# Kernel optimization log

Hardware: AMD Instinct MI355X
Metric: run time of the kernel (lower is better)

## Reference

```python
import math
import jax, jax.numpy as jnp
import numpy as np

CHANNELS = 1024
N_HEADS = 16
WINDOW = 4

def _get_relative_embeddings(emb, length, window):
    # emb: [n_heads_rel, 2*window+1, k_channels]
    pad_len = max(length - (window + 1), 0)
    start = max(window + 1 - length, 0)
    if pad_len > 0:
        emb = jnp.pad(emb, ((0, 0), (pad_len, pad_len), (0, 0)), mode='edge')
    return emb[:, start:start + 2 * length - 1]  # [n_rel, 2L-1, kc]

def _rel_to_abs(x):
    # x: [b, h, t, 2t-1] -> [b, h, t, t] via pad/reshape shift trick
    b, h, t, _ = x.shape
    x = jnp.pad(x, ((0, 0), (0, 0), (0, 0), (0, 1)))          # [b,h,t,2t]
    x = x.reshape(b, h, t * 2 * t)
    x = jnp.pad(x, ((0, 0), (0, 0), (0, t - 1)))
    x = x.reshape(b, h, t + 1, 2 * t - 1)
    return x[:, :, :t, t - 1:]

def setup_inputs() -> dict:
    key = jax.random.key(0)
    ks = jax.random.split(key, 12)
    B, C, T = 8, CHANNELS, 1024
    kc = C // N_HEADS
    sc = 1.0 / math.sqrt(C)
    inp = {
        'x': jax.random.normal(ks[0], (B, C, T), jnp.float32),
        'c': jax.random.normal(ks[1], (B, C, T), jnp.float32),
        'wq': jax.random.normal(ks[2], (C, C), jnp.float32) * sc,
        'bq': jnp.zeros((C,), jnp.float32),
        'wk': jax.random.normal(ks[3], (C, C), jnp.float32) * sc,
        'bk': jnp.zeros((C,), jnp.float32),
        'wv': jax.random.normal(ks[4], (C, C), jnp.float32) * sc,
        'bv': jnp.zeros((C,), jnp.float32),
        'wo': jax.random.normal(ks[5], (C, C), jnp.float32) * sc,
        'bo': jnp.zeros((C,), jnp.float32),
        'emb_rel_k': jax.random.normal(ks[6], (1, 2 * WINDOW + 1, kc), jnp.float32) * kc ** -0.5,
        'emb_rel_v': jax.random.normal(ks[7], (1, 2 * WINDOW + 1, kc), jnp.float32) * kc ** -0.5,
    }
    return inp

def reference(x, c, wq, bq, wk, bk, wv, bv, wo, bo, emb_rel_k, emb_rel_v):
    b, d, t = x.shape
    h = N_HEADS
    kc = d // h
    # 1x1 conv == pointwise linear over channels
    q = jnp.einsum('oc,bct->bot', wq, x) + bq[None, :, None]
    k = jnp.einsum('oc,bct->bot', wk, c) + bk[None, :, None]
    v = jnp.einsum('oc,bct->bot', wv, c) + bv[None, :, None]
    qh = q.reshape(b, h, kc, t)
    kh = k.reshape(b, h, kc, t)
    vh = v.reshape(b, h, kc, t)
    scale = 1.0 / math.sqrt(kc)
    scores = jnp.einsum('bhct,bhcs->bhts', qh * scale, kh)  # [b,h,t,t]
    # relative position bias on keys (heads_share=True -> n_rel=1 broadcast)
    rel_k = _get_relative_embeddings(emb_rel_k, t, WINDOW)  # [1, 2t-1, kc]
    rel_logits = jnp.einsum('bhct,nmc->bhtm', qh * scale, rel_k)  # [b,h,t,2t-1]
    scores = scores + _rel_to_abs(rel_logits)
    p_attn = jax.nn.softmax(scores, axis=-1)
    out = jnp.einsum('bhts,bhcs->bhct', p_attn, vh).reshape(b, d, t)
    out = jnp.einsum('oc,bct->bot', wo, out) + bo[None, :, None]
    return out
```

## Files before the change

kernel.cpp:

```cpp
#include <hip/hip_runtime.h>
#include <stdint.h>


#define DI __device__ __forceinline__

typedef float f32x4 __attribute__((ext_vector_type(4)));
typedef short short4v __attribute__((ext_vector_type(4)));
typedef short short8v __attribute__((ext_vector_type(8)));
typedef int int2v __attribute__((ext_vector_type(2)));
typedef _Float16 f16x4 __attribute__((ext_vector_type(4)));
typedef _Float16 f16x8 __attribute__((ext_vector_type(8)));

DI f32x4 mfma32(short8v a, short8v b, f32x4 c) {
  return __builtin_amdgcn_mfma_f32_16x16x32_f16(
      __builtin_bit_cast(f16x8, a), __builtin_bit_cast(f16x8, b), c, 0, 0, 0);
}
DI f32x4 mfma16x(short4v a, short4v b, f32x4 c) {
  return __builtin_amdgcn_mfma_f32_16x16x16f16(
      __builtin_bit_cast(f16x4, a), __builtin_bit_cast(f16x4, b), c, 0, 0, 0);
}

DI short f2h(float x) {
  _Float16 h = (_Float16)x;
  return __builtin_bit_cast(short, h);
}

DI short4v pack4(float p0, float p1, float p2, float p3) {
  auto a = __builtin_amdgcn_cvt_pkrtz(p0, p1);
  auto b = __builtin_amdgcn_cvt_pkrtz(p2, p3);
  int2v iv;
  iv[0] = __builtin_bit_cast(int, a);
  iv[1] = __builtin_bit_cast(int, b);
  return __builtin_bit_cast(short4v, iv);
}

DI int swz(int r) { return (r ^ (r >> 2)) & 3; }

DI void gl_lds16(const void* g, void* l) {
  __builtin_amdgcn_global_load_lds(
      (const __attribute__((address_space(1))) unsigned int*)g,
      (__attribute__((address_space(3))) unsigned int*)l, 16, 0, 0);
}

__global__ __launch_bounds__(256) void k_pre(
    const float* __restrict__ x, const float* __restrict__ c,
    const float* __restrict__ wq, const float* __restrict__ wk,
    const float* __restrict__ wv, const float* __restrict__ wo,
    short* __restrict__ Wall, short* __restrict__ xT, short* __restrict__ cT) {
  __shared__ float tile[64][65];
  int l = blockIdx.x;
  int tid = threadIdx.x;
  if (l < 4096) {
    int bx = l & 15, by = (l >> 4) & 15, bz = l >> 8;
    const float* src = (bz < 8 ? x : c) + (size_t)(bz & 7) * 1048576;
    short* dst = (bz < 8 ? xT : cT) + (size_t)(bz & 7) * 1048576;
    int t0 = bx * 64, c0 = by * 64;
    int tx = tid & 15, ty = tid >> 4;
#pragma unroll
    for (int rr_ = 0; rr_ < 64; rr_ += 16) {
      int r = rr_ + ty;
      f32x4 v = *(const f32x4*)(src + (size_t)(c0 + r) * 1024 + t0 + tx * 4);
      tile[r][tx * 4 + 0] = v[0]; tile[r][tx * 4 + 1] = v[1];
      tile[r][tx * 4 + 2] = v[2]; tile[r][tx * 4 + 3] = v[3];
    }
    __syncthreads();
#pragma unroll
    for (int rr_ = 0; rr_ < 64; rr_ += 16) {
      int r = rr_ + ty;
      short4v o;
      o[0] = f2h(tile[tx * 4 + 0][r]); o[1] = f2h(tile[tx * 4 + 1][r]);
      o[2] = f2h(tile[tx * 4 + 2][r]); o[3] = f2h(tile[tx * 4 + 3][r]);
      *(short4v*)(dst + (size_t)(t0 + r) * 1024 + c0 + tx * 4) = o;
    }
  } else {
    int l2 = l - 4096;
    int y = l2 >> 10, bx = l2 & 1023;
    const float* src = (y == 0) ? wq : (y == 1) ? wk : (y == 2) ? wv : wo;
    int i = (bx * 256 + tid) * 4;
    f32x4 v = *(const f32x4*)(src + i);
    short4v o;
    o[0] = f2h(v[0]); o[1] = f2h(v[1]); o[2] = f2h(v[2]); o[3] = f2h(v[3]);
    *(short4v*)(Wall + (size_t)y * 1048576 + i) = o;
  }
}

__global__ __launch_bounds__(256, 4) void k_proj(
    const short* __restrict__ Wall, const short* __restrict__ xT,
    const short* __restrict__ cT, const short* __restrict__ aT,
    const float* __restrict__ bq, const float* __restrict__ bk,
    const float* __restrict__ bv, const float* __restrict__ bo,
    short* __restrict__ QT, short* __restrict__ KT, short* __restrict__ Vv,
    float* __restrict__ outO, int zbase) {
  int z = blockIdx.z + zbase;
  int p = z >> 3, b = z & 7;
  const short* W = Wall + (size_t)p * 1048576;
  const short* src;
  const float* bias;
  if (p == 0) { src = xT; bias = bq; }
  else if (p == 1) { src = cT; bias = bk; }
  else if (p == 2) { src = cT; bias = bv; }
  else { src = aT; bias = bo; }
  src += (size_t)b * 1048576;

  int o0 = blockIdx.y * 128, t0 = blockIdx.x * 128;
  __shared__ short lsA[2][4096];
  __shared__ short lsB[2][4096];

  int tid = threadIdx.x;
  int w = tid >> 6, lane = tid & 63, ln = lane & 15, lq = lane >> 4;
  int wm = (w & 1) * 64, wn = (w >> 1) * 64;

  const char* Wb = (const char*)(W + (size_t)o0 * 1024);
  const char* Sb = (const char*)(src + (size_t)t0 * 1024);

  int r0 = tid >> 2, c0ch = tid & 3;
  int r1 = r0 + 64;
  int gO0 = r0 * 2048 + ((c0ch ^ swz(r0)) * 16);
  int gO1 = r1 * 2048 + ((c0ch ^ swz(r1)) * 16);

  f32x4 acc[4][4] = {};

  auto stage = [&](int kk, int bf_) {
    int ko = kk * 64;
    gl_lds16(Wb + gO0 + ko, (char*)lsA[bf_] + (w * 64) * 16);
    gl_lds16(Wb + gO1 + ko, (char*)lsA[bf_] + (256 + w * 64) * 16);
    gl_lds16(Sb + gO0 + ko, (char*)lsB[bf_] + (w * 64) * 16);
    gl_lds16(Sb + gO1 + ko, (char*)lsB[bf_] + (256 + w * 64) * 16);
  };

  stage(0, 0);
  __syncthreads();
  int buf = 0;
#pragma unroll 1
  for (int kk = 0; kk < 32; kk++) {
    if (kk < 31) stage(kk + 1, buf ^ 1);
    short8v af[4], bfr[4];
#pragma unroll
    for (int mt = 0; mt < 4; mt++) {
      int r = wm + mt * 16 + ln;
      af[mt] = *(const short8v*)((const char*)lsA[buf] + r * 64 + ((lq ^ swz(r)) * 16));
    }
#pragma unroll
    for (int nt = 0; nt < 4; nt++) {
      int r = wn + nt * 16 + ln;
      bfr[nt] = *(const short8v*)((const char*)lsB[buf] + r * 64 + ((lq ^ swz(r)) * 16));
    }
#pragma unroll
    for (int mt = 0; mt < 4; mt++)
#pragma unroll
      for (int nt = 0; nt < 4; nt++)
        acc[mt][nt] = mfma32(af[mt], bfr[nt], acc[mt][nt]);
    __syncthreads();
    buf ^= 1;
  }

  if (p == 3) {
    float* ob = outO + (size_t)b * 1048576;
#pragma unroll
    for (int mt = 0; mt < 4; mt++) {
      int ob0 = o0 + wm + mt * 16 + lq * 4;
      f32x4 b4 = *(const f32x4*)(bias + ob0);
#pragma unroll
      for (int nt = 0; nt < 4; nt++) {
        int t = t0 + wn + nt * 16 + ln;
#pragma unroll
        for (int i = 0; i < 4; i++)
          ob[(size_t)(ob0 + i) * 1024 + t] = acc[mt][nt][i] + b4[i];
      }
    }
  } else if (p == 2) {
    short* vb = Vv + (size_t)b * 1048576;
#pragma unroll
    for (int mt = 0; mt < 4; mt++) {
      int ob0 = o0 + wm + mt * 16 + lq * 4;
      f32x4 b4 = *(const f32x4*)(bias + ob0);
#pragma unroll
      for (int nt = 0; nt < 4; nt++) {
        int t = t0 + wn + nt * 16 + ln;
#pragma unroll
        for (int i = 0; i < 4; i++)
          vb[(size_t)(ob0 + i) * 1024 + t] = f2h(acc[mt][nt][i] + b4[i]);
      }
    }
  } else {
    short* dst = (p == 0) ? QT : KT;
    float scale = (p == 0) ? 0.18033688011112042f : 1.0f;
#pragma unroll
    for (int mt = 0; mt < 4; mt++) {
      int ob0 = o0 + wm + mt * 16 + lq * 4;
      int hh = ob0 >> 6, ch = ob0 & 63;
      f32x4 b4 = *(const f32x4*)(bias + ob0);
#pragma unroll
      for (int nt = 0; nt < 4; nt++) {
        int t = t0 + wn + nt * 16 + ln;
        short4v pk;
#pragma unroll
        for (int i = 0; i < 4; i++) pk[i] = f2h((acc[mt][nt][i] + b4[i]) * scale);
        *(short4v*)(dst + ((size_t)(b * 16 + hh) * 1024 + t) * 64 + ch) = pk;
      }
    }
  }
}

#define M_EST 8.5f
__global__ __launch_bounds__(512, 2) void k_attn(
    const short* __restrict__ QT, const short* __restrict__ KT,
    const short* __restrict__ Vv, const float* __restrict__ emb,
    short* __restrict__ attnT) {
  int bh = blockIdx.x;
  int tc = blockIdx.y * 128;
  int tid = threadIdx.x, w = tid >> 6, lane = tid & 63, ln = lane & 15, lq = lane >> 4;
  int t0w = tc + w * 16;

  __shared__ short lsK[3][2048];
  __shared__ short lsV[3][2048];
  __shared__ float lsR[8][16][12];

  const short* Qb = QT + (size_t)bh * 65536;
  const short* Kb = KT + (size_t)bh * 65536;
  const short* Vb = Vv + (size_t)bh * 65536;

  int stid = tid & 255;
  int kr = stid >> 3, kcp = stid & 7;
  int gK = kr * 128 + ((kcp ^ (kr & 7)) * 16);
  int vr = stid >> 2, vcp = stid & 3;
  int gV = vr * 2048 + ((vcp ^ swz(vr)) * 16);
  unsigned ldsb = (unsigned)((w & 3) * 64) * 16;

  auto stageKV = [&](int ss, int bf_) {
    int s0 = ss * 32;
    if (w < 4)
      gl_lds16((const char*)Kb + (size_t)s0 * 128 + gK, (char*)lsK[bf_] + ldsb);
    else
      gl_lds16((const char*)Vb + (size_t)s0 * 2 + gV, (char*)lsV[bf_] + ldsb);
  };

  stageKV(0, 0);

  short8v qf[2];
#pragma unroll
  for (int k2 = 0; k2 < 2; k2++)
    qf[k2] = *(const short8v*)(Qb + (size_t)(t0w + ln) * 64 + k2 * 32 + lq * 8);

  short8v ef[2];
#pragma unroll
  for (int k2 = 0; k2 < 2; k2++) {
    short8v e = {};
    if (ln < 9) {
      const float* ep = emb + ln * 64 + k2 * 32 + lq * 8;
#pragma unroll
      for (int j = 0; j < 8; j++) e[j] = f2h(ep[j]);
    }
    ef[k2] = e;
  }
  {
    f32x4 rt = {};
    rt = mfma32(ef[0], qf[0], rt);
    rt = mfma32(ef[1], qf[1], rt);
#pragma unroll
    for (int i = 0; i < 4; i++) {
      int j = lq * 4 + i;
      if (j < 9) lsR[w][ln][j] = rt[i];
    }
  }
  __syncthreads();
  stageKV(1, 1);
  float rr[9];
#pragma unroll
  for (int j = 0; j < 9; j++) rr[j] = lsR[w][ln][j];

  f32x4 oacc[4] = {};
  float l_run = 0.f;

  int bcur = 0;
#pragma unroll 1
  for (int ss = 0; ss < 32; ss++) {
    if (ss < 31) asm volatile("s_waitcnt vmcnt(1)" ::: "memory");
    else         asm volatile("s_waitcnt vmcnt(0)" ::: "memory");
    asm volatile("s_barrier" ::: "memory");
    if (ss < 30) stageKV(ss + 2, bcur ? bcur - 1 : 2);

    int s0 = ss * 32;
    const char* Kc = (const char*)lsK + bcur * 4096;
    const char* Vc = (const char*)lsV + bcur * 4096;

    float off;
    bool lo = (s0 + 31 <= t0w - 4);
    bool hi = (s0 >= t0w + 19);
    bool band = !(lo || hi);
    if (band) off = M_EST;
    else      off = M_EST - (lo ? rr[0] : rr[8]);

    short8v kf[2][2];
#pragma unroll
    for (int mt = 0; mt < 2; mt++)
#pragma unroll
      for (int k2 = 0; k2 < 2; k2++) {
        int r = mt * 16 + ln;
        kf[mt][k2] = *(const short8v*)(Kc + r * 128 + (((k2 * 4 + lq) ^ (r & 7)) * 16));
      }

    f32x4 st[2];
    __builtin_amdgcn_s_setprio(1);
#pragma unroll
    for (int mt = 0; mt < 2; mt++) {
      f32x4 a = {-off, -off, -off, -off};
      a = mfma32(kf[mt][0], qf[0], a);
      a = mfma32(kf[mt][1], qf[1], a);
      st[mt] = a;
    }
    __builtin_amdgcn_s_setprio(0);

    if (band) {
      int t = t0w + ln;
#pragma unroll
      for (int mt = 0; mt < 2; mt++)
#pragma unroll
        for (int i = 0; i < 4; i++) {
          int d = (s0 + mt * 16 + lq * 4 + i) - t + 4;
          float bb = rr[0];
          bb = (d >= 1) ? rr[1] : bb;
          bb = (d >= 2) ? rr[2] : bb;
          bb = (d >= 3) ? rr[3] : bb;
          bb = (d >= 4) ? rr[4] : bb;
          bb = (d >= 5) ? rr[5] : bb;
          bb = (d >= 6) ? rr[6] : bb;
          bb = (d >= 7) ? rr[7] : bb;
          bb = (d >= 8) ? rr[8] : bb;
          st[mt][i] += bb;
        }
    }

    short4v pf[2];
    {
      float ls = 0.f;
#pragma unroll
      for (int mt = 0; mt < 2; mt++) {
        float p0 = exp2f(st[mt][0]);
        float p1 = exp2f(st[mt][1]);
        float p2 = exp2f(st[mt][2]);
        float p3 = exp2f(st[mt][3]);
        ls += (p0 + p1) + (p2 + p3);
        pf[mt] = pack4(p0, p1, p2, p3);
      }
      l_run += ls;
    }

    __builtin_amdgcn_s_setprio(1);
#pragma unroll
    for (int kt = 0; kt < 2; kt++)
#pragma unroll
      for (int mc4 = 0; mc4 < 4; mc4++) {
        int cr = mc4 * 16 + ln;
        int cpos = (kt * 2 + (lq >> 1)) ^ swz(cr);
        short4v vf = *(const short4v*)(Vc + cr * 64 + cpos * 16 + (lq & 1) * 8);
        oacc[mc4] = mfma16x(vf, pf[kt], oacc[mc4]);
      }
    __builtin_amdgcn_s_setprio(0);

    bcur = (bcur == 2) ? 0 : bcur + 1;
  }

  int b = bh >> 4, h = bh & 15;
  {
    float l = l_run;
    l += __shfl_xor(l, 16, 64);
    l += __shfl_xor(l, 32, 64);
    float inv = 1.f / l;
    int t = t0w + ln;
#pragma unroll
    for (int mc4 = 0; mc4 < 4; mc4++) {
      short4v pk;
      pk[0] = f2h(oacc[mc4][0] * inv);
      pk[1] = f2h(oacc[mc4][1] * inv);
      pk[2] = f2h(oacc[mc4][2] * inv);
      pk[3] = f2h(oacc[mc4][3] * inv);
      *(short4v*)(attnT + ((size_t)(b * 1024 + t)) * 1024 + h * 64 + mc4 * 16 + lq * 4) = pk;
    }
  }
}

extern "C" void kernel_launch(void* const* d_in, const int* in_sizes, int n_in,
                              void* d_out, int out_size, void* d_ws, size_t ws_size,
                              hipStream_t stream) {
  const float* x   = (const float*)d_in[0];
  const float* cc_ = (const float*)d_in[1];
  const float* wq  = (const float*)d_in[2];
  const float* bq  = (const float*)d_in[3];
  const float* wk  = (const float*)d_in[4];
  const float* bk  = (const float*)d_in[5];
  const float* wv  = (const float*)d_in[6];
  const float* bv  = (const float*)d_in[7];
  const float* wo  = (const float*)d_in[8];
  const float* bo  = (const float*)d_in[9];
  const float* emb = (const float*)d_in[10];
  float* out = (float*)d_out;

  short* wsb = (short*)d_ws;
  short* Wall = wsb;
  short* xT = wsb + (size_t)4 * 1048576;
  short* cT = xT + (size_t)8 * 1048576;
  short* QT = cT + (size_t)8 * 1048576;
  short* KT = QT + (size_t)8 * 1048576;
  short* Vv = KT + (size_t)8 * 1048576;
  short* aT = Vv + (size_t)8 * 1048576;

  k_pre<<<dim3(8192), 256, 0, stream>>>(x, cc_, wq, wk, wv, wo, Wall, xT, cT);
  k_proj<<<dim3(8, 8, 24), 256, 0, stream>>>(Wall, xT, cT, aT, bq, bk, bv, bo,
                                             QT, KT, Vv, out, 0);
  k_attn<<<dim3(128, 8), 512, 0, stream>>>(QT, KT, Vv, emb, aT);
  k_proj<<<dim3(8, 8, 8), 256, 0, stream>>>(Wall, xT, cT, aT, bq, bk, bv, bo,
                                            QT, KT, Vv, out, 24);
}
```

Before: 299.4 us.

## Rewrite projection GEMM with 256x256 tiles, 8 waves and split-phase LDS pipeline

Replaces the 128x128 projection GEMM with a 256x256-tile kernel using 512 threads, 128 KB of dynamic LDS, K-step 64, and four half-buffers staged in phases with explicit vmcnt waits and raw barriers. MFMA bursts get raised priority via s_setprio, and the block index is remapped so that neighbouring blocks spread across projections and batches. The goal is higher arithmetic intensity per LDS and global load and better overlap of loads with MFMA. The cost is lower occupancy, far fewer blocks (384 and 128 on a chip with many CUs), and fragile manual wait counts.

```diff
diff --git a/kernel.cpp b/kernel.cpp
--- a/kernel.cpp
+++ b/kernel.cpp
@@ -84,14 +84,21 @@
   }
 }
 
-__global__ __launch_bounds__(256, 4) void k_proj(
+__global__ __launch_bounds__(512, 2) void k_proj256(
     const short* __restrict__ Wall, const short* __restrict__ xT,
     const short* __restrict__ cT, const short* __restrict__ aT,
     const float* __restrict__ bq, const float* __restrict__ bk,
     const float* __restrict__ bv, const float* __restrict__ bo,
     short* __restrict__ QT, short* __restrict__ KT, short* __restrict__ Vv,
     float* __restrict__ outO, int zbase) {
-  int z = blockIdx.z + zbase;
+  extern __shared__ char sm[];
+  int lin = blockIdx.x;
+  int nz = gridDim.x >> 4;
+  int zpx = nz >> 3;
+  int slot = lin >> 3;
+  int zl = (lin & 7) * zpx + (slot >> 4);
+  int tile = slot & 15;
+  int z = zl + zbase;
   int p = z >> 3, b = z & 7;
   const short* W = Wall + (size_t)p * 1048576;
   const short* src;
@@ -102,101 +109,187 @@
   else { src = aT; bias = bo; }
   src += (size_t)b * 1048576;
 
-  int o0 = blockIdx.y * 128, t0 = blockIdx.x * 128;
-  __shared__ short lsA[2][4096];
-  __shared__ short lsB[2][4096];
+  int t0 = (tile & 3) * 256, o0 = (tile >> 2) * 256;
 
   int tid = threadIdx.x;
-  int w = tid >> 6, lane = tid & 63, ln = lane & 15, lq = lane >> 4;
-  int wm = (w & 1) * 64, wn = (w >> 1) * 64;
-
-  const char* Wb = (const char*)(W + (size_t)o0 * 1024);
-  const char* Sb = (const char*)(src + (size_t)t0 * 1024);
-
-  int r0 = tid >> 2, c0ch = tid & 3;
-  int r1 = r0 + 64;
-  int gO0 = r0 * 2048 + ((c0ch ^ swz(r0)) * 16);
-  int gO1 = r1 * 2048 + ((c0ch ^ swz(r1)) * 16);
-
-  f32x4 acc[4][4] = {};
-
-  auto stage = [&](int kk, int bf_) {
-    int ko = kk * 64;
-    gl_lds16(Wb + gO0 + ko, (char*)lsA[bf_] + (w * 64) * 16);
-    gl_lds16(Wb + gO1 + ko, (char*)lsA[bf_] + (256 + w * 64) * 16);
-    gl_lds16(Sb + gO0 + ko, (char*)lsB[bf_] + (w * 64) * 16);
-    gl_lds16(Sb + gO1 + ko, (char*)lsB[bf_] + (256 + w * 64) * 16);
+  int w8 = tid >> 6, l = tid & 63, ln = l & 15, lq = l >> 4;
+  int wm = w8 >> 2, wn = w8 & 3;
+
+  const char* Ga = (const char*)(W + (size_t)o0 * 1024);
+  const char* Gb = (const char*)(src + (size_t)t0 * 1024);
+  char* lsA = sm;
+  char* lsB = sm + 65536;
+
+  int rr0 = (w8 * 2 + 0) * 8 + (l >> 3);
+  int rr1 = (w8 * 2 + 1) * 8 + (l >> 3);
+  int csrc = ((l & 7) ^ ((l >> 3) & 7)) * 16;
+  int gA0[2], gA1[2], gB0[2], gB1[2];
+#pragma unroll
+  for (int r = 0; r < 2; ++r) {
+    gA0[r] = (((rr0 & 63) + ((rr0 & 64) << 1) + r * 64) * 2048) + csrc;
+    gA1[r] = (((rr1 & 63) + ((rr1 & 64) << 1) + r * 64) * 2048) + csrc;
+    gB0[r] = (((rr0 & 31) + ((rr0 >> 5) << 6) + r * 32) * 2048) + csrc;
+    gB1[r] = (((rr1 & 31) + ((rr1 >> 5) << 6) + r * 32) * 2048) + csrc;
+  }
+  unsigned d0 = (unsigned)(w8 * 2 + 0) * 1024 + (unsigned)l * 16;
+  unsigned d1 = (unsigned)(w8 * 2 + 1) * 1024 + (unsigned)l * 16;
+
+  auto STGA = [&](int kt, int bf_, int r) {
+    char* L = lsA + (bf_ * 2 + r) * 16384;
+    gl_lds16(Ga + gA0[r] + kt * 128, L + d0);
+    gl_lds16(Ga + gA1[r] + kt * 128, L + d1);
   };
-
-  stage(0, 0);
-  __syncthreads();
-  int buf = 0;
+  auto STGB = [&](int kt, int bf_, int r) {
+    char* L = lsB + (bf_ * 2 + r) * 16384;
+    gl_lds16(Gb + gB0[r] + kt * 128, L + d0);
+    gl_lds16(Gb + gB1[r] + kt * 128, L + d1);
+  };
+
+  int cswz[2];
+  cswz[0] = (((0 * 4 + lq) ^ (ln & 7)) * 16);
+  cswz[1] = (((1 * 4 + lq) ^ (ln & 7)) * 16);
+  int arow = ln + wm * 64;
+  int brow = ln + wn * 32;
+
+  f32x4 acc[8][4] = {};
+  short8v af[4][2], bf[4][2];
+
+  STGA(0, 0, 0);
+  STGB(0, 0, 0);
+  STGB(0, 0, 1);
+  STGA(0, 0, 1);
+
 #pragma unroll 1
-  for (int kk = 0; kk < 32; kk++) {
-    if (kk < 31) stage(kk + 1, buf ^ 1);
-    short8v af[4], bfr[4];
-#pragma unroll
-    for (int mt = 0; mt < 4; mt++) {
-      int r = wm + mt * 16 + ln;
-      af[mt] = *(const short8v*)((const char*)lsA[buf] + r * 64 + ((lq ^ swz(r)) * 16));
-    }
-#pragma unroll
-    for (int nt = 0; nt < 4; nt++) {
-      int r = wn + nt * 16 + ln;
-      bfr[nt] = *(const short8v*)((const char*)lsB[buf] + r * 64 + ((lq ^ swz(r)) * 16));
-    }
-#pragma unroll
-    for (int mt = 0; mt < 4; mt++)
-#pragma unroll
-      for (int nt = 0; nt < 4; nt++)
-        acc[mt][nt] = mfma32(af[mt], bfr[nt], acc[mt][nt]);
-    __syncthreads();
-    buf ^= 1;
+  for (int t = 0; t < 16; ++t) {
+    int buf = t & 1;
+    const char* Ab0 = lsA + (buf * 2 + 0) * 16384;
+    const char* Ab1 = lsA + (buf * 2 + 1) * 16384;
+    const char* Bb0 = lsB + (buf * 2 + 0) * 16384;
+    const char* Bb1 = lsB + (buf * 2 + 1) * 16384;
+
+    if (t < 15) { STGA(t + 1, buf ^ 1, 0);
+      asm volatile("s_waitcnt vmcnt(6)" ::: "memory");
+    } else {
+      asm volatile("s_waitcnt vmcnt(4)" ::: "memory");
+    }
+    asm volatile("s_barrier" ::: "memory");
+#pragma unroll
+    for (int m = 0; m < 4; ++m) {
+      af[m][0] = *(const short8v*)(Ab0 + (m * 16 + arow) * 128 + cswz[0]);
+      af[m][1] = *(const short8v*)(Ab0 + (m * 16 + arow) * 128 + cswz[1]);
+    }
+#pragma unroll
+    for (int n = 0; n < 2; ++n) {
+      bf[n][0] = *(const short8v*)(Bb0 + ((n & 1) * 16 + brow) * 128 + cswz[0]);
+      bf[n][1] = *(const short8v*)(Bb0 + ((n & 1) * 16 + brow) * 128 + cswz[1]);
+    }
+    __builtin_amdgcn_s_setprio(1);
+#pragma unroll
+    for (int m = 0; m < 4; ++m)
+#pragma unroll
+      for (int n = 0; n < 2; ++n) {
+        acc[m][n] = mfma32(af[m][0], bf[n][0], acc[m][n]);
+        acc[m][n] = mfma32(af[m][1], bf[n][1], acc[m][n]);
+      }
+    __builtin_amdgcn_s_setprio(0);
+
+    if (t < 15) { STGB(t + 1, buf ^ 1, 0);
+      asm volatile("s_waitcnt vmcnt(6)" ::: "memory");
+    } else {
+      asm volatile("s_waitcnt vmcnt(2)" ::: "memory");
+    }
+    asm volatile("s_barrier" ::: "memory");
+#pragma unroll
+    for (int n = 2; n < 4; ++n) {
+      bf[n][0] = *(const short8v*)(Bb1 + ((n & 1) * 16 + brow) * 128 + cswz[0]);
+      bf[n][1] = *(const short8v*)(Bb1 + ((n & 1) * 16 + brow) * 128 + cswz[1]);
+    }
+    __builtin_amdgcn_s_setprio(1);
+#pragma unroll
+    for (int m = 0; m < 4; ++m)
+#pragma unroll
+      for (int n = 2; n < 4; ++n) {
+        acc[m][n] = mfma32(af[m][0], bf[n][0], acc[m][n]);
+        acc[m][n] = mfma32(af[m][1], bf[n][1], acc[m][n]);
+      }
+    __builtin_amdgcn_s_setprio(0);
+
+    if (t < 15) { STGB(t + 1, buf ^ 1, 1);
+      asm volatile("s_waitcnt vmcnt(6)" ::: "memory");
+    } else {
+      asm volatile("s_waitcnt vmcnt(0)" ::: "memory");
+    }
+    asm volatile("s_barrier" ::: "memory");
+#pragma unroll
+    for (int m = 0; m < 4; ++m) {
+      af[m][0] = *(const short8v*)(Ab1 + (m * 16 + arow) * 128 + cswz[0]);
+      af[m][1] = *(const short8v*)(Ab1 + (m * 16 + arow) * 128 + cswz[1]);
+    }
+    __builtin_amdgcn_s_setprio(1);
+#pragma unroll
+    for (int m = 0; m < 4; ++m)
+#pragma unroll
+      for (int n = 0; n < 2; ++n) {
+        acc[4 + m][n] = mfma32(af[m][0], bf[n][0], acc[4 + m][n]);
+        acc[4 + m][n] = mfma32(af[m][1], bf[n][1], acc[4 + m][n]);
+      }
+    __builtin_amdgcn_s_setprio(0);
+
+    if (t < 15) STGA(t + 1, buf ^ 1, 1);
+    __builtin_amdgcn_s_setprio(1);
+#pragma unroll
+    for (int m = 0; m < 4; ++m)
+#pragma unroll
+      for (int n = 2; n < 4; ++n) {
+        acc[4 + m][n] = mfma32(af[m][0], bf[n][0], acc[4 + m][n]);
+        acc[4 + m][n] = mfma32(af[m][1], bf[n][1], acc[4 + m][n]);
+      }
+    __builtin_amdgcn_s_setprio(0);
   }
 
   if (p == 3) {
     float* ob = outO + (size_t)b * 1048576;
 #pragma unroll
-    for (int mt = 0; mt < 4; mt++) {
-      int ob0 = o0 + wm + mt * 16 + lq * 4;
+    for (int m = 0; m < 8; ++m) {
+      int ob0 = o0 + wm * 128 + m * 16 + lq * 4;
       f32x4 b4 = *(const f32x4*)(bias + ob0);
 #pragma unroll
-      for (int nt = 0; nt < 4; nt++) {
-        int t = t0 + wn + nt * 16 + ln;
-#pragma unroll
-        for (int i = 0; i < 4; i++)
-          ob[(size_t)(ob0 + i) * 1024 + t] = acc[mt][nt][i] + b4[i];
+      for (int n = 0; n < 4; ++n) {
+        int tt = t0 + wn * 64 + n * 16 + ln;
+#pragma unroll
+        for (int i = 0; i < 4; ++i)
+          ob[(size_t)(ob0 + i) * 1024 + tt] = acc[m][n][i] + b4[i];
       }
     }
   } else if (p == 2) {
     short* vb = Vv + (size_t)b * 1048576;
 #pragma unroll
-    for (int mt = 0; mt < 4; mt++) {
-      int ob0 = o0 + wm + mt * 16 + lq * 4;
+    for (int m = 0; m < 8; ++m) {
+      int ob0 = o0 + wm * 128 + m * 16 + lq * 4;
       f32x4 b4 = *(const f32x4*)(bias + ob0);
 #pragma unroll
-      for (int nt = 0; nt < 4; nt++) {
-        int t = t0 + wn + nt * 16 + ln;
-#pragma unroll
-        for (int i = 0; i < 4; i++)
-          vb[(size_t)(ob0 + i) * 1024 + t] = f2h(acc[mt][nt][i] + b4[i]);
+      for (int n = 0; n < 4; ++n) {
+        int tt = t0 + wn * 64 + n * 16 + ln;
+#pragma unroll
+        for (int i = 0; i < 4; ++i)
+          vb[(size_t)(ob0 + i) * 1024 + tt] = f2h(acc[m][n][i] + b4[i]);
       }
     }
   } else {
     short* dst = (p == 0) ? QT : KT;
     float scale = (p == 0) ? 0.18033688011112042f : 1.0f;
 #pragma unroll
-    for (int mt = 0; mt < 4; mt++) {
-      int ob0 = o0 + wm + mt * 16 + lq * 4;
+    for (int m = 0; m < 8; ++m) {
+      int ob0 = o0 + wm * 128 + m * 16 + lq * 4;
       int hh = ob0 >> 6, ch = ob0 & 63;
       f32x4 b4 = *(const f32x4*)(bias + ob0);
 #pragma unroll
-      for (int nt = 0; nt < 4; nt++) {
-        int t = t0 + wn + nt * 16 + ln;
+      for (int n = 0; n < 4; ++n) {
+        int tt = t0 + wn * 64 + n * 16 + ln;
         short4v pk;
 #pragma unroll
-        for (int i = 0; i < 4; i++) pk[i] = f2h((acc[mt][nt][i] + b4[i]) * scale);
-        *(short4v*)(dst + ((size_t)(b * 16 + hh) * 1024 + t) * 64 + ch) = pk;
+        for (int i = 0; i < 4; ++i) pk[i] = f2h((acc[m][n][i] + b4[i]) * scale);
+        *(short4v*)(dst + ((size_t)(b * 16 + hh) * 1024 + tt) * 64 + ch) = pk;
       }
     }
   }
@@ -405,10 +498,17 @@
   short* Vv = KT + (size_t)8 * 1048576;
   short* aT = Vv + (size_t)8 * 1048576;
 
+  static bool attr_set = false;
+  if (!attr_set) {
+    hipFuncSetAttribute(reinterpret_cast<const void*>(k_proj256),
+                        hipFuncAttributeMaxDynamicSharedMemorySize, 131072);
+    attr_set = true;
+  }
+
   k_pre<<<dim3(8192), 256, 0, stream>>>(x, cc_, wq, wk, wv, wo, Wall, xT, cT);
-  k_proj<<<dim3(8, 8, 24), 256, 0, stream>>>(Wall, xT, cT, aT, bq, bk, bv, bo,
-                                             QT, KT, Vv, out, 0);
+  k_proj256<<<dim3(384), 512, 131072, stream>>>(Wall, xT, cT, aT, bq, bk, bv, bo,
+                                                QT, KT, Vv, out, 0);
   k_attn<<<dim3(128, 8), 512, 0, stream>>>(QT, KT, Vv, emb, aT);
-  k_proj<<<dim3(8, 8, 8), 256, 0, stream>>>(Wall, xT, cT, aT, bq, bk, bv, bo,
-                                            QT, KT, Vv, out, 24);
-}
+  k_proj256<<<dim3(128), 512, 131072, stream>>>(Wall, xT, cT, aT, bq, bk, bv, bo,
+                                                QT, KT, Vv, out, 24);
+}
```

New measurement: 316.3 us. 5.6% more time.
